# Kernel tuning notes

Hardware: AMD Instinct MI355X
Metric: run time of the kernel (lower is better)

The kernel has to match this reference:

```python
import jax, jax.numpy as jnp
import numpy as np

B, TXT, REF, IMG = 1, 512, 512, 1536
DIM, H, D = 3072, 24, 128
S = REF + IMG            # hidden_states tokens (ref + img)
STOT = TXT + S           # full sequence [txt, ref, img]
EPS = 1e-6


def setup_inputs() -> dict:
    key = jax.random.key(0)
    ks = jax.random.split(key, 16)
    p = lambda k, sh: jax.random.normal(k, sh, jnp.float32) * 0.02
    return {
        "hidden_states": jax.random.normal(ks[0], (B, S, DIM), jnp.float32),
        "encoder_hidden_states": jax.random.normal(ks[1], (B, TXT, DIM), jnp.float32),
        "rope_cos": jax.random.uniform(ks[2], (STOT, D), jnp.float32),
        "rope_sin": jax.random.uniform(ks[3], (STOT, D), jnp.float32),
        "wq": p(ks[4], (DIM, H * D)), "bq": jnp.zeros((H * D,), jnp.float32),
        "wk": p(ks[5], (DIM, H * D)), "bk": jnp.zeros((H * D,), jnp.float32),
        "wv": p(ks[6], (DIM, H * D)), "bv": jnp.zeros((H * D,), jnp.float32),
        "waq": p(ks[7], (DIM, H * D)), "baq": jnp.zeros((H * D,), jnp.float32),
        "wak": p(ks[8], (DIM, H * D)), "bak": jnp.zeros((H * D,), jnp.float32),
        "wav": p(ks[9], (DIM, H * D)), "bav": jnp.zeros((H * D,), jnp.float32),
        "nq": jnp.ones((D,), jnp.float32), "nk": jnp.ones((D,), jnp.float32),
        "naq": jnp.ones((D,), jnp.float32), "nak": jnp.ones((D,), jnp.float32),
        "wo": p(ks[10], (H * D, DIM)), "bo": jnp.zeros((DIM,), jnp.float32),
        "wao": p(ks[11], (H * D, DIM)), "bao": jnp.zeros((DIM,), jnp.float32),
        "num_ref_tokens": REF,
    }


def _rms(x, w):
    # per-head RMSNorm over head_dim (diffusers RMSNorm, eps=1e-6)
    return x * jax.lax.rsqrt(jnp.mean(x * x, axis=-1, keepdims=True) + EPS) * w


def _rope(x, cos, sin):
    # diffusers apply_rotary_emb use_real=True, interleaved pairs; x: [B,S,H,D]
    xp = x.reshape(x.shape[:-1] + (D // 2, 2))
    rot = jnp.stack([-xp[..., 1], xp[..., 0]], axis=-1).reshape(x.shape)
    return x * cos[None, :, None, :] + rot * sin[None, :, None, :]


def _sdpa(q, k, v):
    # q,k,v: [B,S,H,D] diffusers convention
    scale = 1.0 / np.float32(np.sqrt(D))
    s = jnp.einsum('bqhd,bkhd->bhqk', q, k) * scale
    p = jax.nn.softmax(s, axis=-1)
    return jnp.einsum('bhqk,bkhd->bqhd', p, v)


def reference(hidden_states, encoder_hidden_states, rope_cos, rope_sin,
              wq, bq, wk, bk, wv, bv, waq, baq, wak, bak, wav, bav,
              nq, nk, naq, nak, wo, bo, wao, bao, num_ref_tokens):
    b, s, _ = hidden_states.shape
    txt = encoder_hidden_states.shape[1]
    # QKV projections for ref+img stream
    q = (hidden_states @ wq + bq).reshape(b, s, H, D)
    k = (hidden_states @ wk + bk).reshape(b, s, H, D)
    v = (hidden_states @ wv + bv).reshape(b, s, H, D)
    q = _rms(q, nq)
    k = _rms(k, nk)
    # added (txt) projections
    eq = (encoder_hidden_states @ waq + baq).reshape(b, txt, H, D)
    ek = (encoder_hidden_states @ wak + bak).reshape(b, txt, H, D)
    ev = (encoder_hidden_states @ wav + bav).reshape(b, txt, H, D)
    eq = _rms(eq, naq)
    ek = _rms(ek, nak)
    # sequence layout [txt, ref, img]
    query = jnp.concatenate([eq, q], axis=1)
    key = jnp.concatenate([ek, k], axis=1)
    value = jnp.concatenate([ev, v], axis=1)
    query = _rope(query, rope_cos, rope_sin)
    key = _rope(key, rope_cos, rope_sin)
    # structured attention (extract mode): ref tokens self-attend only,
    # txt+img tokens attend to everything
    ref_start = txt
    ref_end = txt + num_ref_tokens
    q_ti = jnp.concatenate([query[:, :ref_start], query[:, ref_end:]], axis=1)
    attn_ti = _sdpa(q_ti, key, value)
    attn_ref = _sdpa(query[:, ref_start:ref_end],
                     key[:, ref_start:ref_end],
                     value[:, ref_start:ref_end])
    out = jnp.concatenate([attn_ti[:, :ref_start], attn_ref, attn_ti[:, ref_start:]],
                          axis=1).reshape(b, txt + s, H * D)
    enc_out = out[:, :txt] @ wao + bao
    hs_out = out[:, txt:] @ wo + bo
    return (hs_out, enc_out)
```

## Files before the change

kernel.cpp:

```cpp
#include <hip/hip_runtime.h>
#include <hip/hip_bf16.h>

typedef unsigned short u16;
typedef unsigned int u32;
typedef __bf16 bf16x8 __attribute__((ext_vector_type(8)));
typedef float f32x4 __attribute__((ext_vector_type(4)));
typedef unsigned int u32x4 __attribute__((ext_vector_type(4)));
typedef unsigned int u32x2 __attribute__((ext_vector_type(2)));

#define TXT 512
#define SEQ 2048
#define STOT 2560
#define DIM 3072
#define NH 24
#define HD 128
#define SOFTMAX_SCALE 0.08838834764831845f

typedef const __attribute__((address_space(1))) void gas_void;
typedef __attribute__((address_space(3))) void las_void;

__device__ __forceinline__ float b2f(u16 u) {
    union { u32 i; float f; } c; c.i = ((u32)u) << 16; return c.f;
}
__device__ __forceinline__ u16 f2b(float f) {
    union { float f; u32 i; } c; c.f = f;
    u32 x = c.i;
    return (u16)((x + 0x7FFFu + ((x >> 16) & 1u)) >> 16);
}
__device__ __forceinline__ u32 pk2(float a, float b) {
    __hip_bfloat162 h = __float22bfloat162_rn(make_float2(a, b));
    return *reinterpret_cast<u32*>(&h);
}
__device__ __forceinline__ f32x4 max4(f32x4 a, f32x4 b) {
    return (f32x4){fmaxf(a[0], b[0]), fmaxf(a[1], b[1]),
                   fmaxf(a[2], b[2]), fmaxf(a[3], b[3])};
}
__device__ __forceinline__ f32x4 shfl_xor4(f32x4 v, int mask) {
    return (f32x4){__shfl_xor(v[0], mask), __shfl_xor(v[1], mask),
                   __shfl_xor(v[2], mask), __shfl_xor(v[3], mask)};
}

__global__ __launch_bounds__(256) void convert_bf16_kernel(
    const float* __restrict__ src, u16* __restrict__ dst, int n8)
{
    int i = blockIdx.x * 256 + threadIdx.x;
    if (i < n8) {
        const f32x4* p = reinterpret_cast<const f32x4*>(src + (size_t)i * 8);
        f32x4 a = p[0], b = p[1];
        u32x4 o = {pk2(a[0], a[1]), pk2(a[2], a[3]), pk2(b[0], b[1]), pk2(b[2], b[3])};
        *reinterpret_cast<u32x4*>(dst + (size_t)i * 8) = o;
    }
}

__global__ __launch_bounds__(256, 2) void transpose_w_kernel(
    const float* __restrict__ W, u16* __restrict__ WT,
    int K, int Ntot, int nbase)
{
    __shared__ u16 Ts[64][66];
    const int t   = threadIdx.x;
    const int k0  = blockIdx.x * 64;
    const int n0l = blockIdx.y * 64;
    const int n0g = nbase + n0l;

    {
        const int krow = t >> 2;
        const int nseg = (t & 3) * 16;
        const float* src = &W[(size_t)(k0 + krow) * Ntot + n0g + nseg];
        f32x4 v0 = reinterpret_cast<const f32x4*>(src)[0];
        f32x4 v1 = reinterpret_cast<const f32x4*>(src)[1];
        f32x4 v2 = reinterpret_cast<const f32x4*>(src)[2];
        f32x4 v3 = reinterpret_cast<const f32x4*>(src)[3];
        #pragma unroll
        for (int i = 0; i < 4; i++) Ts[nseg +      i][krow] = f2b(v0[i]);
        #pragma unroll
        for (int i = 0; i < 4; i++) Ts[nseg +  4 + i][krow] = f2b(v1[i]);
        #pragma unroll
        for (int i = 0; i < 4; i++) Ts[nseg +  8 + i][krow] = f2b(v2[i]);
        #pragma unroll
        for (int i = 0; i < 4; i++) Ts[nseg + 12 + i][krow] = f2b(v3[i]);
    }
    __syncthreads();
    {
        const int nrow = t >> 2;
        const int kseg = (t & 3) * 16;
        u32 out[8];
        #pragma unroll
        for (int c = 0; c < 8; c++)
            out[c] = (u32)Ts[nrow][kseg + 2 * c] | ((u32)Ts[nrow][kseg + 2 * c + 1] << 16);
        u16* dst = &WT[(size_t)(n0l + nrow) * K + k0 + kseg];
        *reinterpret_cast<u32x4*>(dst)     = (u32x4){out[0], out[1], out[2], out[3]};
        *reinterpret_cast<u32x4*>(dst + 8) = (u32x4){out[4], out[5], out[6], out[7]};
    }
}

template<int OUTMODE, int MT>
__global__ __launch_bounds__(256, 2) void gemm_bt2_kernel(
    const u16* __restrict__ A, const u16* __restrict__ BT,
    const float* __restrict__ bias, void* __restrict__ Cv, size_t coff,
    int K, int Ntot, int ncol0)
{
    constexpr int MI  = MT / 32;
    constexpr int ASP = MT / 32;
    __shared__ __align__(16) u16 As[MT][64];
    __shared__ __align__(16) u16 Bs[128][64];

    const int t    = threadIdx.x;
    const int lane = t & 63;
    const int wave = t >> 6;
    const int wr   = wave >> 1;
    const int wc   = wave & 1;
    const int m0   = blockIdx.x * MT;
    const int n0   = blockIdx.y * 128;
    const int fm   = lane & 15;
    const int fq   = lane >> 4;

    const int srow = t >> 3;
    const int skb  = (t & 7) * 8;

    f32x4 acc[MI][4];
    #pragma unroll
    for (int i = 0; i < MI; i++)
        #pragma unroll
        for (int j = 0; j < 4; j++)
            acc[i][j] = (f32x4){0.f, 0.f, 0.f, 0.f};

    const u16* aBase = A  + (size_t)(m0 + srow) * K + skb;
    const u16* bBase = BT + (size_t)(n0 + srow) * K + skb;
    char* asDst = (char*)&As[0][0] + (size_t)wave * 1024;
    char* bsDst = (char*)&Bs[0][0] + (size_t)wave * 1024;

    for (int k0 = 0; k0 < K; k0 += 64) {
        __syncthreads();
        #pragma unroll
        for (int s = 0; s < 4; s++)
            __builtin_amdgcn_global_load_lds(
                (gas_void*)(bBase + (size_t)(s * 32) * K + k0),
                (las_void*)(bsDst + s * 4096), 16, 0, 0);
        #pragma unroll
        for (int s = 0; s < ASP; s++)
            __builtin_amdgcn_global_load_lds(
                (gas_void*)(aBase + (size_t)(s * 32) * K + k0),
                (las_void*)(asDst + s * 4096), 16, 0, 0);
        __syncthreads();

        #pragma unroll
        for (int h = 0; h < 2; h++) {
            bf16x8 af[MI], bfr[4];
            #pragma unroll
            for (int i = 0; i < MI; i++)
                af[i] = *reinterpret_cast<const bf16x8*>(
                    &As[wr * (MT / 2) + i * 16 + fm][h * 32 + fq * 8]);
            #pragma unroll
            for (int j = 0; j < 4; j++)
                bfr[j] = *reinterpret_cast<const bf16x8*>(
                    &Bs[wc * 64 + j * 16 + fm][h * 32 + fq * 8]);
            #pragma unroll
            for (int i = 0; i < MI; i++)
                #pragma unroll
                for (int j = 0; j < 4; j++)
                    acc[i][j] = __builtin_amdgcn_mfma_f32_16x16x32_bf16(af[i], bfr[j], acc[i][j], 0, 0, 0);
        }
    }

    #pragma unroll
    for (int i = 0; i < MI; i++) {
        #pragma unroll
        for (int j = 0; j < 4; j++) {
            int col = ncol0 + n0 + wc * 64 + j * 16 + fm;
            float bb = bias[col];
            if (OUTMODE == 2) {
                int tok = (int)coff + m0 + wr * (MT / 2) + i * 16 + fq * 4;
                u32x2 pr = {pk2(acc[i][j][0] + bb, acc[i][j][1] + bb),
                            pk2(acc[i][j][2] + bb, acc[i][j][3] + bb)};
                *reinterpret_cast<u32x2*>(&((u16*)Cv)[(size_t)col * STOT + tok]) = pr;
            } else {
                #pragma unroll
                for (int r = 0; r < 4; r++) {
                    int row = m0 + wr * (MT / 2) + i * 16 + fq * 4 + r;
                    size_t idx = coff + (size_t)row * Ntot + col;
                    float val = acc[i][j][r] + bb;
                    if (OUTMODE == 1) ((float*)Cv)[idx] = val;
                    else              ((u16*)Cv)[idx]   = f2b(val);
                }
            }
        }
    }
}

template<int AF32, int OUTMODE, int MT>
__global__ __launch_bounds__(256, 2) void gemm_bt_kernel(
    const void* __restrict__ Av, const u16* __restrict__ BT,
    const float* __restrict__ bias, void* __restrict__ Cv, size_t coff,
    int M, int K, int Ntot, int ncol0)
{
    constexpr int MI = MT / 32;
    constexpr int ASEGN = (MT == 128) ? 32 : 16;
    __shared__ u16 As[MT][72];
    __shared__ u16 Bs[128][72];

    const int t    = threadIdx.x;
    const int lane = t & 63;
    const int wave = t >> 6;
    const int wr   = wave >> 1;
    const int wc   = wave & 1;
    const int m0   = blockIdx.x * MT;
    const int n0   = blockIdx.y * 128;
    const int fm   = lane & 15;
    const int fq   = lane >> 4;

    const int arow = (MT == 128) ? (t >> 1) : (t >> 2);
    const int aseg = (MT == 128) ? ((t & 1) * 32) : ((t & 3) * 16);
    const int brow = t >> 1;
    const int bseg = (t & 1) * 32;

    f32x4 acc[MI][4];
    #pragma unroll
    for (int i = 0; i < MI; i++)
        #pragma unroll
        for (int j = 0; j < 4; j++)
            acc[i][j] = (f32x4){0.f, 0.f, 0.f, 0.f};

    for (int k0 = 0; k0 < K; k0 += 64) {
        u32 aw[ASEGN / 2];
        if (AF32) {
            const float* ap = (const float*)Av + (size_t)(m0 + arow) * K + k0 + aseg;
            #pragma unroll
            for (int c = 0; c < ASEGN / 4; c++) {
                f32x4 x = reinterpret_cast<const f32x4*>(ap)[c];
                aw[2 * c]     = pk2(x[0], x[1]);
                aw[2 * c + 1] = pk2(x[2], x[3]);
            }
        } else {
            const u32x4* ap = reinterpret_cast<const u32x4*>(
                (const u16*)Av + (size_t)(m0 + arow) * K + k0 + aseg);
            #pragma unroll
            for (int c = 0; c < ASEGN / 8; c++) {
                u32x4 x = ap[c];
                aw[4 * c] = x[0]; aw[4 * c + 1] = x[1];
                aw[4 * c + 2] = x[2]; aw[4 * c + 3] = x[3];
            }
        }
        u32x4 bw[4];
        {
            const u32x4* bp = reinterpret_cast<const u32x4*>(
                &BT[(size_t)(n0 + brow) * K + k0 + bseg]);
            bw[0] = bp[0]; bw[1] = bp[1]; bw[2] = bp[2]; bw[3] = bp[3];
        }
        __syncthreads();
        #pragma unroll
        for (int c = 0; c < ASEGN / 8; c++)
            *reinterpret_cast<u32x4*>(&As[arow][aseg + c * 8]) =
                (u32x4){aw[4 * c], aw[4 * c + 1], aw[4 * c + 2], aw[4 * c + 3]};
        #pragma unroll
        for (int c = 0; c < 4; c++)
            *reinterpret_cast<u32x4*>(&Bs[brow][bseg + c * 8]) = bw[c];
        __syncthreads();

        #pragma unroll
        for (int h = 0; h < 2; h++) {
            bf16x8 af[MI], bfr[4];
            #pragma unroll
            for (int i = 0; i < MI; i++)
                af[i] = *reinterpret_cast<const bf16x8*>(
                    &As[wr * (MT / 2) + i * 16 + fm][h * 32 + fq * 8]);
            #pragma unroll
            for (int j = 0; j < 4; j++)
                bfr[j] = *reinterpret_cast<const bf16x8*>(
                    &Bs[wc * 64 + j * 16 + fm][h * 32 + fq * 8]);
            #pragma unroll
            for (int i = 0; i < MI; i++)
                #pragma unroll
                for (int j = 0; j < 4; j++)
                    acc[i][j] = __builtin_amdgcn_mfma_f32_16x16x32_bf16(af[i], bfr[j], acc[i][j], 0, 0, 0);
        }
    }

    #pragma unroll
    for (int i = 0; i < MI; i++) {
        #pragma unroll
        for (int j = 0; j < 4; j++) {
            int col = ncol0 + n0 + wc * 64 + j * 16 + fm;
            float bb = bias[col];
            if (OUTMODE == 2) {
                int tok = (int)coff + m0 + wr * (MT / 2) + i * 16 + fq * 4;
                u32x2 pr = {pk2(acc[i][j][0] + bb, acc[i][j][1] + bb),
                            pk2(acc[i][j][2] + bb, acc[i][j][3] + bb)};
                *reinterpret_cast<u32x2*>(&((u16*)Cv)[(size_t)col * STOT + tok]) = pr;
            } else {
                #pragma unroll
                for (int r = 0; r < 4; r++) {
                    int row = m0 + wr * (MT / 2) + i * 16 + fq * 4 + r;
                    size_t idx = coff + (size_t)row * Ntot + col;
                    float val = acc[i][j][r] + bb;
                    if (OUTMODE == 1) ((float*)Cv)[idx] = val;
                    else              ((u16*)Cv)[idx]   = f2b(val);
                }
            }
        }
    }
}

template<int AF32, int OUTMODE>
__global__ __launch_bounds__(256, 2) void gemm_bias_kernel(
    const void* __restrict__ Av, const float* __restrict__ W,
    const float* __restrict__ bias, void* __restrict__ Cv, size_t coff,
    int M, int K, int N)
{
    __shared__ u16 As[128][40];
    __shared__ u16 Bs[128][40];

    const int t    = threadIdx.x;
    const int lane = t & 63;
    const int wave = t >> 6;
    const int wr   = wave >> 1;
    const int wc   = wave & 1;
    const int m0   = blockIdx.x * 128;
    const int n0   = blockIdx.y * 128;
    const int fm   = lane & 15;
    const int fq   = lane >> 4;

    const int arow = t >> 1;
    const int akg  = (t & 1) * 16;
    const int bn   = t >> 1;
    const int bkg  = (t & 1) * 16;

    f32x4 acc[4][4];
    #pragma unroll
    for (int i = 0; i < 4; i++)
        #pragma unroll
        for (int j = 0; j < 4; j++)
            acc[i][j] = (f32x4){0.f, 0.f, 0.f, 0.f};

    for (int k0 = 0; k0 < K; k0 += 32) {
        u32x4 a0, a1;
        if (AF32) {
            const f32x4* p = reinterpret_cast<const f32x4*>(
                (const float*)Av + (size_t)(m0 + arow) * K + k0 + akg);
            f32x4 x0 = p[0], x1 = p[1], x2 = p[2], x3 = p[3];
            a0 = (u32x4){pk2(x0[0], x0[1]), pk2(x0[2], x0[3]),
                         pk2(x1[0], x1[1]), pk2(x1[2], x1[3])};
            a1 = (u32x4){pk2(x2[0], x2[1]), pk2(x2[2], x2[3]),
                         pk2(x3[0], x3[1]), pk2(x3[2], x3[3])};
        } else {
            const u32x4* p = reinterpret_cast<const u32x4*>(
                (const u16*)Av + (size_t)(m0 + arow) * K + k0 + akg);
            a0 = p[0]; a1 = p[1];
        }
        float wv[16];
        #pragma unroll
        for (int j = 0; j < 16; j++)
            wv[j] = W[(size_t)(k0 + bkg + j) * N + n0 + bn];
        u32x4 b0, b1;
        #pragma unroll
        for (int j = 0; j < 4; j++) {
            b0[j] = pk2(wv[2 * j],     wv[2 * j + 1]);
            b1[j] = pk2(wv[8 + 2 * j], wv[8 + 2 * j + 1]);
        }
        __syncthreads();
        *reinterpret_cast<u32x4*>(&As[arow][akg])     = a0;
        *reinterpret_cast<u32x4*>(&As[arow][akg + 8]) = a1;
        *reinterpret_cast<u32x4*>(&Bs[bn][bkg])       = b0;
        *reinterpret_cast<u32x4*>(&Bs[bn][bkg + 8])   = b1;
        __syncthreads();

        bf16x8 af[4], bfr[4];
        #pragma unroll
        for (int i = 0; i < 4; i++)
            af[i] = *reinterpret_cast<const bf16x8*>(&As[wr * 64 + i * 16 + fm][fq * 8]);
        #pragma unroll
        for (int j = 0; j < 4; j++)
            bfr[j] = *reinterpret_cast<const bf16x8*>(&Bs[wc * 64 + j * 16 + fm][fq * 8]);
        #pragma unroll
        for (int i = 0; i < 4; i++)
            #pragma unroll
            for (int j = 0; j < 4; j++)
                acc[i][j] = __builtin_amdgcn_mfma_f32_16x16x32_bf16(af[i], bfr[j], acc[i][j], 0, 0, 0);
    }

    #pragma unroll
    for (int i = 0; i < 4; i++) {
        #pragma unroll
        for (int j = 0; j < 4; j++) {
            int col = n0 + wc * 64 + j * 16 + fm;
            float bb = bias[col];
            if (OUTMODE == 2) {
                int tok = (int)coff + m0 + wr * 64 + i * 16 + fq * 4;
                u32x2 pr = {pk2(acc[i][j][0] + bb, acc[i][j][1] + bb),
                            pk2(acc[i][j][2] + bb, acc[i][j][3] + bb)};
                *reinterpret_cast<u32x2*>(&((u16*)Cv)[(size_t)col * STOT + tok]) = pr;
            } else {
                #pragma unroll
                for (int r = 0; r < 4; r++) {
                    int row = m0 + wr * 64 + i * 16 + fq * 4 + r;
                    size_t idx = coff + (size_t)row * N + col;
                    float val = acc[i][j][r] + bb;
                    if (OUTMODE == 1) ((float*)Cv)[idx] = val;
                    else              ((u16*)Cv)[idx]   = f2b(val);
                }
            }
        }
    }
}

__global__ __launch_bounds__(256) void rmsrope_kernel(
    u16* __restrict__ Qf, u16* __restrict__ Kf,
    const float* __restrict__ nq, const float* __restrict__ nk,
    const float* __restrict__ naq, const float* __restrict__ nak,
    const float* __restrict__ cosb, const float* __restrict__ sinb)
{
    const int h     = blockIdx.x;
    const int tok   = blockIdx.y * 4 + (threadIdx.x >> 6);
    const int which = blockIdx.z;
    u16* buf = which ? Kf : Qf;
    const float* nw = (tok < TXT) ? (which ? nak : naq) : (which ? nk : nq);
    const int t = threadIdx.x & 63;
    const size_t base = (size_t)tok * DIM + h * HD + 2 * t;

    u32 pr = *reinterpret_cast<const u32*>(&buf[base]);
    float x0 = b2f((u16)(pr & 0xFFFF));
    float x1 = b2f((u16)(pr >> 16));

    float ss = x0 * x0 + x1 * x1;
    #pragma unroll
    for (int off = 32; off; off >>= 1) ss += __shfl_xor(ss, off);
    float r = rsqrtf(ss * (1.0f / 128.0f) + 1e-6f);

    float y0 = x0 * r * nw[2 * t];
    float y1 = x1 * r * nw[2 * t + 1];
    float c0 = cosb[tok * HD + 2 * t];
    float c1 = cosb[tok * HD + 2 * t + 1];
    float s0 = sinb[tok * HD + 2 * t];
    float s1 = sinb[tok * HD + 2 * t + 1];
    float o0 = y0 * c0 - y1 * s0;
    float o1 = y1 * c1 + y0 * s1;
    *reinterpret_cast<u32*>(&buf[base]) = pk2(o0, o1);
}

__global__ __launch_bounds__(256, 2) void attn_kernel(
    const u16* __restrict__ Qf, const u16* __restrict__ Kf,
    const u16* __restrict__ VTg, u16* __restrict__ AO)
{
    __shared__ u16 Ks[64][136];
    __shared__ u16 VTs[128][72];
    __shared__ u16 Ps[4][32][72];

    const int t    = threadIdx.x;
    const int w    = t >> 6;
    const int lane = t & 63;
    const int col  = lane & 15;
    const int quad = lane >> 4;

    const int flat = blockIdx.x + blockIdx.y * 20;
    const int rm   = (flat & 7) * 60 + (flat >> 3);
    const int h    = rm / 20;
    const int q0   = (rm % 20) * 128;

    const bool is_ref = (q0 >= TXT) && (q0 < TXT + 512);
    const int ks = is_ref ? TXT : 0;
    const int ke = is_ref ? (TXT + 512) : STOT;

    bf16x8 Qfrag[2][4];
    #pragma unroll
    for (int s = 0; s < 2; s++) {
        const size_t qbase = (size_t)(q0 + w * 32 + s * 16 + col) * DIM + h * HD;
        #pragma unroll
        for (int c = 0; c < 4; c++)
            Qfrag[s][c] = *reinterpret_cast<const bf16x8*>(&Qf[qbase + c * 32 + quad * 8]);
    }

    f32x4 O[2][8];
    f32x4 m[2], l[2];
    #pragma unroll
    for (int s = 0; s < 2; s++) {
        #pragma unroll
        for (int dt = 0; dt < 8; dt++) O[s][dt] = (f32x4){0.f, 0.f, 0.f, 0.f};
        m[s] = (f32x4){-1e30f, -1e30f, -1e30f, -1e30f};
        l[s] = (f32x4){0.f, 0.f, 0.f, 0.f};
    }

    const int krow = t >> 2, kseg = t & 3;
    const int vrow = t >> 1, vseg = t & 1;

    u32x4 kreg[4], vreg[4];
    {
        const u32x4* src = reinterpret_cast<const u32x4*>(
            &Kf[(size_t)(ks + krow) * DIM + h * HD + kseg * 32]);
        kreg[0] = src[0]; kreg[1] = src[1]; kreg[2] = src[2]; kreg[3] = src[3];
        const u32x4* vsrc = reinterpret_cast<const u32x4*>(
            &VTg[(size_t)(h * HD + vrow) * STOT + ks + vseg * 32]);
        vreg[0] = vsrc[0]; vreg[1] = vsrc[1]; vreg[2] = vsrc[2]; vreg[3] = vsrc[3];
    }

    for (int k0 = ks; k0 < ke; k0 += 64) {
        __syncthreads();
        {
            u32x4* dst = reinterpret_cast<u32x4*>(&Ks[krow][kseg * 32]);
            dst[0] = kreg[0]; dst[1] = kreg[1]; dst[2] = kreg[2]; dst[3] = kreg[3];
            u32x4* vdst = reinterpret_cast<u32x4*>(&VTs[vrow][vseg * 32]);
            vdst[0] = vreg[0]; vdst[1] = vreg[1]; vdst[2] = vreg[2]; vdst[3] = vreg[3];
        }
        __syncthreads();

        if (k0 + 64 < ke) {
            const u32x4* src = reinterpret_cast<const u32x4*>(
                &Kf[(size_t)(k0 + 64 + krow) * DIM + h * HD + kseg * 32]);
            kreg[0] = src[0]; kreg[1] = src[1]; kreg[2] = src[2]; kreg[3] = src[3];
            const u32x4* vsrc = reinterpret_cast<const u32x4*>(
                &VTg[(size_t)(h * HD + vrow) * STOT + k0 + 64 + vseg * 32]);
            vreg[0] = vsrc[0]; vreg[1] = vsrc[1]; vreg[2] = vsrc[2]; vreg[3] = vsrc[3];
        }

        f32x4 sc[2][4];
        #pragma unroll
        for (int kt = 0; kt < 4; kt++) {
            f32x4 a0 = (f32x4){0.f, 0.f, 0.f, 0.f};
            f32x4 a1 = (f32x4){0.f, 0.f, 0.f, 0.f};
            #pragma unroll
            for (int c = 0; c < 4; c++) {
                bf16x8 kf = *reinterpret_cast<const bf16x8*>(
                    &Ks[kt * 16 + col][c * 32 + quad * 8]);
                a0 = __builtin_amdgcn_mfma_f32_16x16x32_bf16(Qfrag[0][c], kf, a0, 0, 0, 0);
                a1 = __builtin_amdgcn_mfma_f32_16x16x32_bf16(Qfrag[1][c], kf, a1, 0, 0, 0);
            }
            sc[0][kt] = a0 * SOFTMAX_SCALE;
            sc[1][kt] = a1 * SOFTMAX_SCALE;
        }

        #pragma unroll
        for (int s = 0; s < 2; s++) {
            f32x4 tmax = max4(max4(sc[s][0], sc[s][1]), max4(sc[s][2], sc[s][3]));
            tmax = max4(tmax, shfl_xor4(tmax, 1));
            tmax = max4(tmax, shfl_xor4(tmax, 2));
            tmax = max4(tmax, shfl_xor4(tmax, 4));
            tmax = max4(tmax, shfl_xor4(tmax, 8));
            const bool ok = (tmax[0] - m[s][0] <= 8.0f) && (tmax[1] - m[s][1] <= 8.0f) &&
                            (tmax[2] - m[s][2] <= 8.0f) && (tmax[3] - m[s][3] <= 8.0f);
            const bool skip = __all(ok);
            f32x4 mnew = skip ? m[s] : max4(m[s], tmax);

            f32x4 rowsum = (f32x4){0.f, 0.f, 0.f, 0.f};
            f32x4 p[4];
            #pragma unroll
            for (int kt = 0; kt < 4; kt++)
                #pragma unroll
                for (int r = 0; r < 4; r++) {
                    p[kt][r] = __expf(sc[s][kt][r] - mnew[r]);
                    rowsum[r] += p[kt][r];
                }
            rowsum += shfl_xor4(rowsum, 1);
            rowsum += shfl_xor4(rowsum, 2);
            rowsum += shfl_xor4(rowsum, 4);
            rowsum += shfl_xor4(rowsum, 8);

            if (skip) {
                #pragma unroll
                for (int r = 0; r < 4; r++) l[s][r] += rowsum[r];
            } else {
                f32x4 alpha;
                #pragma unroll
                for (int r = 0; r < 4; r++) alpha[r] = __expf(m[s][r] - mnew[r]);
                #pragma unroll
                for (int r = 0; r < 4; r++) l[s][r] = l[s][r] * alpha[r] + rowsum[r];
                m[s] = mnew;
                #pragma unroll
                for (int dt = 0; dt < 8; dt++)
                    #pragma unroll
                    for (int r = 0; r < 4; r++) O[s][dt][r] *= alpha[r];
            }

            #pragma unroll
            for (int r = 0; r < 4; r++) {
                u32 w01 = pk2(p[0][r], p[1][r]);
                u32 w23 = pk2(p[2][r], p[3][r]);
                u16* prow = &Ps[w][s * 16 + quad * 4 + r][0];
                prow[col]      = (u16)(w01 & 0xFFFFu);
                prow[col + 16] = (u16)(w01 >> 16);
                prow[col + 32] = (u16)(w23 & 0xFFFFu);
                prow[col + 48] = (u16)(w23 >> 16);
            }
        }

        __builtin_amdgcn_s_setprio(1);
        #pragma unroll
        for (int c = 0; c < 2; c++) {
            bf16x8 pf0 = *reinterpret_cast<const bf16x8*>(
                &Ps[w][col][c * 32 + quad * 8]);
            bf16x8 pf1 = *reinterpret_cast<const bf16x8*>(
                &Ps[w][16 + col][c * 32 + quad * 8]);
            #pragma unroll
            for (int dt = 0; dt < 8; dt++) {
                bf16x8 vf = *reinterpret_cast<const bf16x8*>(
                    &VTs[dt * 16 + col][c * 32 + quad * 8]);
                O[0][dt] = __builtin_amdgcn_mfma_f32_16x16x32_bf16(pf0, vf, O[0][dt], 0, 0, 0);
                O[1][dt] = __builtin_amdgcn_mfma_f32_16x16x32_bf16(pf1, vf, O[1][dt], 0, 0, 0);
            }
        }
        __builtin_amdgcn_s_setprio(0);
    }

    #pragma unroll
    for (int s = 0; s < 2; s++) {
        f32x4 inv;
        #pragma unroll
        for (int r = 0; r < 4; r++) inv[r] = 1.0f / l[s][r];
        #pragma unroll
        for (int dt = 0; dt < 8; dt++)
            #pragma unroll
            for (int r = 0; r < 4; r++)
                AO[(size_t)(q0 + w * 32 + s * 16 + quad * 4 + r) * DIM + h * HD + dt * 16 + col] =
                    f2b(O[s][dt][r] * inv[r]);
    }
}

extern "C" void kernel_launch(void* const* d_in, const int* in_sizes, int n_in,
                              void* d_out, int out_size, void* d_ws, size_t ws_size,
                              hipStream_t stream)
{
    const void*  hs  = d_in[0];
    const void*  enc = d_in[1];
    const float* rc  = (const float*)d_in[2];
    const float* rs  = (const float*)d_in[3];
    const float* wq  = (const float*)d_in[4];  const float* bq  = (const float*)d_in[5];
    const float* wk  = (const float*)d_in[6];  const float* bk  = (const float*)d_in[7];
    const float* wv  = (const float*)d_in[8];  const float* bv  = (const float*)d_in[9];
    const float* waq = (const float*)d_in[10]; const float* baq = (const float*)d_in[11];
    const float* wak = (const float*)d_in[12]; const float* bak = (const float*)d_in[13];
    const float* wav = (const float*)d_in[14]; const float* bav = (const float*)d_in[15];
    const float* nq  = (const float*)d_in[16]; const float* nk  = (const float*)d_in[17];
    const float* naq = (const float*)d_in[18]; const float* nak = (const float*)d_in[19];
    const float* wo  = (const float*)d_in[20]; const float* bo  = (const float*)d_in[21];
    const float* wao = (const float*)d_in[22]; const float* bao = (const float*)d_in[23];

    const size_t QFB = (size_t)STOT * DIM * sizeof(u16);
    const size_t WTF = (size_t)DIM * DIM * sizeof(u16);
    u16* Qf  = (u16*)d_ws;
    u16* WT  = (u16*)((char*)d_ws + QFB);
    u16* Xbf = (u16*)((char*)d_ws + QFB + WTF);
    u16* Kf  = (u16*)d_out;
    u16* VTg = (u16*)d_out + (size_t)STOT * DIM;
    u16* AO  = Qf;

    dim3 blk(256);
    dim3 tgrid(DIM / 64, DIM / 64);

    if (ws_size >= 2 * QFB + WTF) {
        convert_bf16_kernel<<<dim3((SEQ * DIM / 8) / 256), blk, 0, stream>>>(
            (const float*)hs, Xbf + (size_t)TXT * DIM, SEQ * DIM / 8);
        convert_bf16_kernel<<<dim3((TXT * DIM / 8) / 256), blk, 0, stream>>>(
            (const float*)enc, Xbf, TXT * DIM / 8);
        #define RUN2(MODE_, MT_, Aptr, Wptr, Bias, Cptr, Coff, M_)                   \
            transpose_w_kernel<<<tgrid, blk, 0, stream>>>(Wptr, WT, DIM, DIM, 0);    \
            gemm_bt2_kernel<MODE_, MT_><<<dim3((M_) / MT_, DIM / 128), blk, 0, stream>>>( \
                Aptr, WT, Bias, Cptr, Coff, DIM, DIM, 0);
        RUN2(0, 128, Xbf + (size_t)TXT * DIM, wq,  bq,  Qf,  (size_t)TXT * DIM, SEQ)
        RUN2(0, 128, Xbf + (size_t)TXT * DIM, wk,  bk,  Kf,  (size_t)TXT * DIM, SEQ)
        RUN2(2, 128, Xbf + (size_t)TXT * DIM, wv,  bv,  VTg, (size_t)TXT,       SEQ)
        RUN2(0, 64,  Xbf,                     waq, baq, Qf,  0,                 TXT)
        RUN2(0, 64,  Xbf,                     wak, bak, Kf,  0,                 TXT)
        RUN2(2, 64,  Xbf,                     wav, bav, VTg, 0,                 TXT)
        rmsrope_kernel<<<dim3(NH, STOT / 4, 2), blk, 0, stream>>>(Qf, Kf, nq, nk, naq, nak, rc, rs);
        attn_kernel<<<dim3(STOT / 128, NH), blk, 0, stream>>>(Qf, Kf, VTg, AO);
        RUN2(1, 128, AO + (size_t)TXT * DIM, wo,  bo,  d_out, 0,                 SEQ)
        RUN2(1, 64,  AO,                     wao, bao, d_out, (size_t)SEQ * DIM, TXT)
        #undef RUN2
        return;
    }

    int nchunk;
    if      (ws_size >= QFB + WTF)     nchunk = DIM;
    else if (ws_size >= QFB + WTF / 2) nchunk = DIM / 2;
    else                               nchunk = 0;

    if (nchunk > 0) {
        dim3 tgrid2(DIM / 64, nchunk / 64);
        #define RUN_GEMM(AF32_, MODE_, MT_, Aptr, Wptr, Bias, Cptr, Coff, M_)     \
            for (int nb = 0; nb < DIM; nb += nchunk) {                            \
                transpose_w_kernel<<<tgrid2, blk, 0, stream>>>(Wptr, WT, DIM, DIM, nb); \
                gemm_bt_kernel<AF32_, MODE_, MT_><<<dim3((M_) / MT_, nchunk / 128), blk, 0, stream>>>( \
                    Aptr, WT, Bias, Cptr, Coff, M_, DIM, DIM, nb);                \
            }
        RUN_GEMM(1, 0, 128, hs,  wq,  bq,  Qf,  (size_t)TXT * DIM, SEQ)
        RUN_GEMM(1, 0, 128, hs,  wk,  bk,  Kf,  (size_t)TXT * DIM, SEQ)
        RUN_GEMM(1, 2, 128, hs,  wv,  bv,  VTg, (size_t)TXT,       SEQ)
        RUN_GEMM(1, 0, 64,  enc, waq, baq, Qf,  0,                 TXT)
        RUN_GEMM(1, 0, 64,  enc, wak, bak, Kf,  0,                 TXT)
        RUN_GEMM(1, 2, 64,  enc, wav, bav, VTg, 0,                 TXT)
        rmsrope_kernel<<<dim3(NH, STOT / 4, 2), blk, 0, stream>>>(Qf, Kf, nq, nk, naq, nak, rc, rs);
        attn_kernel<<<dim3(STOT / 128, NH), blk, 0, stream>>>(Qf, Kf, VTg, AO);
        RUN_GEMM(0, 1, 128, AO + (size_t)TXT * DIM, wo,  bo,  d_out, 0,                 SEQ)
        RUN_GEMM(0, 1, 64,  AO,                     wao, bao, d_out, (size_t)SEQ * DIM, TXT)
        #undef RUN_GEMM
    } else {
        gemm_bias_kernel<1,0><<<dim3(SEQ / 128, DIM / 128), blk, 0, stream>>>(hs, wq, bq, Qf, (size_t)TXT * DIM, SEQ, DIM, DIM);
        gemm_bias_kernel<1,0><<<dim3(SEQ / 128, DIM / 128), blk, 0, stream>>>(hs, wk, bk, Kf, (size_t)TXT * DIM, SEQ, DIM, DIM);
        gemm_bias_kernel<1,2><<<dim3(SEQ / 128, DIM / 128), blk, 0, stream>>>(hs, wv, bv, VTg, (size_t)TXT, SEQ, DIM, DIM);
        gemm_bias_kernel<1,0><<<dim3(TXT / 128, DIM / 128), blk, 0, stream>>>(enc, waq, baq, Qf, 0, TXT, DIM, DIM);
        gemm_bias_kernel<1,0><<<dim3(TXT / 128, DIM / 128), blk, 0, stream>>>(enc, wak, bak, Kf, 0, TXT, DIM, DIM);
        gemm_bias_kernel<1,2><<<dim3(TXT / 128, DIM / 128), blk, 0, stream>>>(enc, wav, bav, VTg, 0, TXT, DIM, DIM);
        rmsrope_kernel<<<dim3(NH, STOT / 4, 2), blk, 0, stream>>>(Qf, Kf, nq, nk, naq, nak, rc, rs);
        attn_kernel<<<dim3(STOT / 128, NH), blk, 0, stream>>>(Qf, Kf, VTg, AO);
        gemm_bias_kernel<0,1><<<dim3(SEQ / 128, DIM / 128), blk, 0, stream>>>(AO + (size_t)TXT * DIM, wo, bo, d_out, 0, SEQ, DIM, DIM);
        gemm_bias_kernel<0,1><<<dim3(TXT / 128, DIM / 128), blk, 0, stream>>>(AO, wao, bao, d_out, (size_t)SEQ * DIM, TXT, DIM, DIM);
    }
}
```

Measured before the change: 1.033 ms.

## Fuse Q and K projections into one wide GEMM with interleaved QK buffer

Adds a new path for when the workspace is large enough. It transposes both the Q and K weights up front and runs a single GEMM of width 2*DIM that writes an interleaved QK buffer. V and the txt-side V are batched into one weight staging step, and the output projections share staging the same way. rmsrope and attention gain a row-stride parameter so they can read the interleaved layout. The aim is fewer kernel launches, better GPU fill from the wider N, and less weight transposing. In exchange it needs a larger workspace and leaves the A-operand load pattern unchanged.

```diff
diff --git a/kernel.cpp b/kernel.cpp
--- a/kernel.cpp
+++ b/kernel.cpp
@@ -403,7 +403,7 @@
 }
 
 __global__ __launch_bounds__(256) void rmsrope_kernel(
-    u16* __restrict__ Qf, u16* __restrict__ Kf,
+    u16* __restrict__ Qb, u16* __restrict__ Kb, int qks,
     const float* __restrict__ nq, const float* __restrict__ nk,
     const float* __restrict__ naq, const float* __restrict__ nak,
     const float* __restrict__ cosb, const float* __restrict__ sinb)
@@ -411,10 +411,10 @@
     const int h     = blockIdx.x;
     const int tok   = blockIdx.y * 4 + (threadIdx.x >> 6);
     const int which = blockIdx.z;
-    u16* buf = which ? Kf : Qf;
+    u16* buf = which ? Kb : Qb;
     const float* nw = (tok < TXT) ? (which ? nak : naq) : (which ? nk : nq);
     const int t = threadIdx.x & 63;
-    const size_t base = (size_t)tok * DIM + h * HD + 2 * t;
+    const size_t base = (size_t)tok * qks + h * HD + 2 * t;
 
     u32 pr = *reinterpret_cast<const u32*>(&buf[base]);
     float x0 = b2f((u16)(pr & 0xFFFF));
@@ -437,7 +437,7 @@
 }
 
 __global__ __launch_bounds__(256, 2) void attn_kernel(
-    const u16* __restrict__ Qf, const u16* __restrict__ Kf,
+    const u16* __restrict__ Qb, const u16* __restrict__ Kb, int qks,
     const u16* __restrict__ VTg, u16* __restrict__ AO)
 {
     __shared__ u16 Ks[64][136];
@@ -462,10 +462,10 @@
     bf16x8 Qfrag[2][4];
     #pragma unroll
     for (int s = 0; s < 2; s++) {
-        const size_t qbase = (size_t)(q0 + w * 32 + s * 16 + col) * DIM + h * HD;
+        const size_t qbase = (size_t)(q0 + w * 32 + s * 16 + col) * qks + h * HD;
         #pragma unroll
         for (int c = 0; c < 4; c++)
-            Qfrag[s][c] = *reinterpret_cast<const bf16x8*>(&Qf[qbase + c * 32 + quad * 8]);
+            Qfrag[s][c] = *reinterpret_cast<const bf16x8*>(&Qb[qbase + c * 32 + quad * 8]);
     }
 
     f32x4 O[2][8];
@@ -484,7 +484,7 @@
     u32x4 kreg[4], vreg[4];
     {
         const u32x4* src = reinterpret_cast<const u32x4*>(
-            &Kf[(size_t)(ks + krow) * DIM + h * HD + kseg * 32]);
+            &Kb[(size_t)(ks + krow) * qks + h * HD + kseg * 32]);
         kreg[0] = src[0]; kreg[1] = src[1]; kreg[2] = src[2]; kreg[3] = src[3];
         const u32x4* vsrc = reinterpret_cast<const u32x4*>(
             &VTg[(size_t)(h * HD + vrow) * STOT + ks + vseg * 32]);
@@ -503,7 +503,7 @@
 
         if (k0 + 64 < ke) {
             const u32x4* src = reinterpret_cast<const u32x4*>(
-                &Kf[(size_t)(k0 + 64 + krow) * DIM + h * HD + kseg * 32]);
+                &Kb[(size_t)(k0 + 64 + krow) * qks + h * HD + kseg * 32]);
             kreg[0] = src[0]; kreg[1] = src[1]; kreg[2] = src[2]; kreg[3] = src[3];
             const u32x4* vsrc = reinterpret_cast<const u32x4*>(
                 &VTg[(size_t)(h * HD + vrow) * STOT + k0 + 64 + vseg * 32]);
@@ -633,17 +633,67 @@
 
     const size_t QFB = (size_t)STOT * DIM * sizeof(u16);
     const size_t WTF = (size_t)DIM * DIM * sizeof(u16);
+    const size_t DD  = (size_t)DIM * DIM;
+
+    dim3 blk(256);
+    dim3 tgrid(DIM / 64, DIM / 64);
+
+    if (ws_size >= 2 * QFB + 3 * WTF) {
+        u16*   QK2  = (u16*)d_ws;
+        u16*   WT2  = (u16*)((char*)d_ws + 31457280);
+        u16*   AOa  = (u16*)((char*)d_ws + 69206016);
+        float* bQK  = (float*)((char*)d_ws + 84934656);
+        float* bQKa = (float*)((char*)d_ws + 84959232);
+        u16*   VTg  = (u16*)d_out;
+        u16*   Xbf  = (u16*)d_out + (size_t)STOT * DIM;
+
+        convert_bf16_kernel<<<dim3((SEQ * DIM / 8) / 256), blk, 0, stream>>>(
+            (const float*)hs, Xbf + (size_t)TXT * DIM, SEQ * DIM / 8);
+        convert_bf16_kernel<<<dim3((TXT * DIM / 8) / 256), blk, 0, stream>>>(
+            (const float*)enc, Xbf, TXT * DIM / 8);
+        hipMemcpyAsync(bQK,         bq,  DIM * sizeof(float), hipMemcpyDeviceToDevice, stream);
+        hipMemcpyAsync(bQK + DIM,   bk,  DIM * sizeof(float), hipMemcpyDeviceToDevice, stream);
+        hipMemcpyAsync(bQKa,        baq, DIM * sizeof(float), hipMemcpyDeviceToDevice, stream);
+        hipMemcpyAsync(bQKa + DIM,  bak, DIM * sizeof(float), hipMemcpyDeviceToDevice, stream);
+
+        transpose_w_kernel<<<tgrid, blk, 0, stream>>>(wq, WT2,      DIM, DIM, 0);
+        transpose_w_kernel<<<tgrid, blk, 0, stream>>>(wk, WT2 + DD, DIM, DIM, 0);
+        gemm_bt2_kernel<0, 128><<<dim3(SEQ / 128, 2 * DIM / 128), blk, 0, stream>>>(
+            Xbf + (size_t)TXT * DIM, WT2, bQK, QK2, (size_t)TXT * 2 * DIM, DIM, 2 * DIM, 0);
+        transpose_w_kernel<<<tgrid, blk, 0, stream>>>(waq, WT2,      DIM, DIM, 0);
+        transpose_w_kernel<<<tgrid, blk, 0, stream>>>(wak, WT2 + DD, DIM, DIM, 0);
+        gemm_bt2_kernel<0, 64><<<dim3(TXT / 64, 2 * DIM / 128), blk, 0, stream>>>(
+            Xbf, WT2, bQKa, QK2, 0, DIM, 2 * DIM, 0);
+
+        transpose_w_kernel<<<tgrid, blk, 0, stream>>>(wv,  WT2,      DIM, DIM, 0);
+        transpose_w_kernel<<<tgrid, blk, 0, stream>>>(wav, WT2 + DD, DIM, DIM, 0);
+        gemm_bt2_kernel<2, 128><<<dim3(SEQ / 128, DIM / 128), blk, 0, stream>>>(
+            Xbf + (size_t)TXT * DIM, WT2,      bv,  VTg, (size_t)TXT, DIM, DIM, 0);
+        gemm_bt2_kernel<2, 64><<<dim3(TXT / 64, DIM / 128), blk, 0, stream>>>(
+            Xbf,                     WT2 + DD, bav, VTg, 0,           DIM, DIM, 0);
+
+        rmsrope_kernel<<<dim3(NH, STOT / 4, 2), blk, 0, stream>>>(
+            QK2, QK2 + DIM, 2 * DIM, nq, nk, naq, nak, rc, rs);
+        attn_kernel<<<dim3(STOT / 128, NH), blk, 0, stream>>>(
+            QK2, QK2 + DIM, 2 * DIM, VTg, AOa);
+
+        transpose_w_kernel<<<tgrid, blk, 0, stream>>>(wo,  WT2,      DIM, DIM, 0);
+        transpose_w_kernel<<<tgrid, blk, 0, stream>>>(wao, WT2 + DD, DIM, DIM, 0);
+        gemm_bt2_kernel<1, 128><<<dim3(SEQ / 128, DIM / 128), blk, 0, stream>>>(
+            AOa + (size_t)TXT * DIM, WT2,      bo,  d_out, 0,                 DIM, DIM, 0);
+        gemm_bt2_kernel<1, 64><<<dim3(TXT / 64, DIM / 128), blk, 0, stream>>>(
+            AOa,                     WT2 + DD, bao, d_out, (size_t)SEQ * DIM, DIM, DIM, 0);
+        return;
+    }
+
     u16* Qf  = (u16*)d_ws;
-    u16* WT  = (u16*)((char*)d_ws + QFB);
-    u16* Xbf = (u16*)((char*)d_ws + QFB + WTF);
     u16* Kf  = (u16*)d_out;
     u16* VTg = (u16*)d_out + (size_t)STOT * DIM;
     u16* AO  = Qf;
 
-    dim3 blk(256);
-    dim3 tgrid(DIM / 64, DIM / 64);
-
     if (ws_size >= 2 * QFB + WTF) {
+        u16* WT  = (u16*)((char*)d_ws + QFB);
+        u16* Xbf = (u16*)((char*)d_ws + QFB + WTF);
         convert_bf16_kernel<<<dim3((SEQ * DIM / 8) / 256), blk, 0, stream>>>(
             (const float*)hs, Xbf + (size_t)TXT * DIM, SEQ * DIM / 8);
         convert_bf16_kernel<<<dim3((TXT * DIM / 8) / 256), blk, 0, stream>>>(
@@ -658,8 +708,8 @@
         RUN2(0, 64,  Xbf,                     waq, baq, Qf,  0,                 TXT)
         RUN2(0, 64,  Xbf,                     wak, bak, Kf,  0,                 TXT)
         RUN2(2, 64,  Xbf,                     wav, bav, VTg, 0,                 TXT)
-        rmsrope_kernel<<<dim3(NH, STOT / 4, 2), blk, 0, stream>>>(Qf, Kf, nq, nk, naq, nak, rc, rs);
-        attn_kernel<<<dim3(STOT / 128, NH), blk, 0, stream>>>(Qf, Kf, VTg, AO);
+        rmsrope_kernel<<<dim3(NH, STOT / 4, 2), blk, 0, stream>>>(Qf, Kf, DIM, nq, nk, naq, nak, rc, rs);
+        attn_kernel<<<dim3(STOT / 128, NH), blk, 0, stream>>>(Qf, Kf, DIM, VTg, AO);
         RUN2(1, 128, AO + (size_t)TXT * DIM, wo,  bo,  d_out, 0,                 SEQ)
         RUN2(1, 64,  AO,                     wao, bao, d_out, (size_t)SEQ * DIM, TXT)
         #undef RUN2
@@ -672,6 +722,7 @@
     else                               nchunk = 0;
 
     if (nchunk > 0) {
+        u16* WT = (u16*)((char*)d_ws + QFB);
         dim3 tgrid2(DIM / 64, nchunk / 64);
         #define RUN_GEMM(AF32_, MODE_, MT_, Aptr, Wptr, Bias, Cptr, Coff, M_)     \
             for (int nb = 0; nb < DIM; nb += nchunk) {                            \
@@ -685,8 +736,8 @@
         RUN_GEMM(1, 0, 64,  enc, waq, baq, Qf,  0,                 TXT)
         RUN_GEMM(1, 0, 64,  enc, wak, bak, Kf,  0,                 TXT)
         RUN_GEMM(1, 2, 64,  enc, wav, bav, VTg, 0,                 TXT)
-        rmsrope_kernel<<<dim3(NH, STOT / 4, 2), blk, 0, stream>>>(Qf, Kf, nq, nk, naq, nak, rc, rs);
-        attn_kernel<<<dim3(STOT / 128, NH), blk, 0, stream>>>(Qf, Kf, VTg, AO);
+        rmsrope_kernel<<<dim3(NH, STOT / 4, 2), blk, 0, stream>>>(Qf, Kf, DIM, nq, nk, naq, nak, rc, rs);
+        attn_kernel<<<dim3(STOT / 128, NH), blk, 0, stream>>>(Qf, Kf, DIM, VTg, AO);
         RUN_GEMM(0, 1, 128, AO + (size_t)TXT * DIM, wo,  bo,  d_out, 0,                 SEQ)
         RUN_GEMM(0, 1, 64,  AO,                     wao, bao, d_out, (size_t)SEQ * DIM, TXT)
         #undef RUN_GEMM
@@ -697,8 +748,8 @@
         gemm_bias_kernel<1,0><<<dim3(TXT / 128, DIM / 128), blk, 0, stream>>>(enc, waq, baq, Qf, 0, TXT, DIM, DIM);
         gemm_bias_kernel<1,0><<<dim3(TXT / 128, DIM / 128), blk, 0, stream>>>(enc, wak, bak, Kf, 0, TXT, DIM, DIM);
         gemm_bias_kernel<1,2><<<dim3(TXT / 128, DIM / 128), blk, 0, stream>>>(enc, wav, bav, VTg, 0, TXT, DIM, DIM);
-        rmsrope_kernel<<<dim3(NH, STOT / 4, 2), blk, 0, stream>>>(Qf, Kf, nq, nk, naq, nak, rc, rs);
-        attn_kernel<<<dim3(STOT / 128, NH), blk, 0, stream>>>(Qf, Kf, VTg, AO);
+        rmsrope_kernel<<<dim3(NH, STOT / 4, 2), blk, 0, stream>>>(Qf, Kf, DIM, nq, nk, naq, nak, rc, rs);
+        attn_kernel<<<dim3(STOT / 128, NH), blk, 0, stream>>>(Qf, Kf, DIM, VTg, AO);
         gemm_bias_kernel<0,1><<<dim3(SEQ / 128, DIM / 128), blk, 0, stream>>>(AO + (size_t)TXT * DIM, wo, bo, d_out, 0, SEQ, DIM, DIM);
         gemm_bias_kernel<0,1><<<dim3(TXT / 128, DIM / 128), blk, 0, stream>>>(AO, wao, bao, d_out, (size_t)SEQ * DIM, TXT, DIM, DIM);
     }
```

After: 951.3 us. 1.09x faster.
